# Kernel optimization log

Measured on AMD Instinct MI355X. Metric: run time of the kernel, lower is better.

## Reference

```python
import jax, jax.numpy as jnp
import numpy as np

B, N, DIM, HEADS, FFN, H, W = 8, 100, 256, 8, 2048, 128, 128
M = H * W
HD = DIM // HEADS
EPS = 1e-5


def ln(x, g, b):
    mu = jnp.mean(x, axis=-1, keepdims=True)
    var = jnp.mean(jnp.square(x - mu), axis=-1, keepdims=True)
    return (x - mu) * jax.lax.rsqrt(var + EPS) * g + b


def setup_inputs() -> dict:
    key = jax.random.key(0)
    ks = jax.random.split(key, 20)
    w = lambda k, shape: jax.random.normal(k, shape, jnp.float32) * 0.02
    inp = {
        "x": jax.random.normal(ks[0], (B, N, DIM), jnp.float32),
        "context": jax.random.normal(ks[1], (B, M, DIM), jnp.float32),
        "mask": jax.random.randint(ks[2], (B, N, H, W), 0, 2, jnp.int32),
        # masked cross-attention params
        "mq_w": w(ks[3], (DIM, DIM)), "mq_b": jnp.zeros((DIM,), jnp.float32),
        "mkv_w": w(ks[4], (2 * DIM, DIM)), "mkv_b": jnp.zeros((2 * DIM,), jnp.float32),
        "mproj_w": w(ks[5], (DIM, DIM)), "mproj_b": jnp.zeros((DIM,), jnp.float32),
        # nn.MultiheadAttention params
        "in_w": w(ks[6], (3 * DIM, DIM)), "in_b": jnp.zeros((3 * DIM,), jnp.float32),
        "out_w": w(ks[7], (DIM, DIM)), "out_b": jnp.zeros((DIM,), jnp.float32),
        # FFN params
        "w1": w(ks[8], (FFN, DIM)), "b1": jnp.zeros((FFN,), jnp.float32),
        "w2": w(ks[9], (DIM, FFN)), "b2": jnp.zeros((DIM,), jnp.float32),
        # LayerNorm params
        "n1_g": jnp.ones((DIM,), jnp.float32), "n1_b": jnp.zeros((DIM,), jnp.float32),
        "n2_g": jnp.ones((DIM,), jnp.float32), "n2_b": jnp.zeros((DIM,), jnp.float32),
        "n3_g": jnp.ones((DIM,), jnp.float32), "n3_b": jnp.zeros((DIM,), jnp.float32),
        "n4_g": jnp.ones((DIM,), jnp.float32), "n4_b": jnp.zeros((DIM,), jnp.float32),
    }
    return inp


def reference(x, context, mask, mq_w, mq_b, mkv_w, mkv_b, mproj_w, mproj_b,
              in_w, in_b, out_w, out_b, w1, b1, w2, b2,
              n1_g, n1_b, n2_g, n2_b, n3_g, n3_b, n4_g, n4_b):
    b, n, _ = x.shape
    m = context.shape[1]
    scale = HD ** -0.5

    # ---- masked cross-attention (pre-norm1, residual) ----
    res = x
    y = ln(x, n1_g, n1_b)
    q = (y @ mq_w.T + mq_b).reshape(b, n, HEADS, HD).transpose(0, 2, 1, 3)        # [b,h,n,d]
    kv = (context @ mkv_w.T + mkv_b).reshape(b, m, 2, HEADS, HD)
    k = kv[:, :, 0].transpose(0, 2, 1, 3)                                         # [b,h,m,d]
    v = kv[:, :, 1].transpose(0, 2, 1, 3)
    dots = jnp.einsum('bhnd,bhmd->bhnm', q, k) * scale                            # [b,h,n,m]
    mflat = mask.reshape(b, n, m)[:, None]                                        # [b,1,n,m]
    dots = jnp.where(mflat == 0, -jnp.inf, dots)
    attn = jax.nn.softmax(dots, axis=-1)
    o = jnp.einsum('bhnm,bhmd->bhnd', attn, v).transpose(0, 2, 1, 3).reshape(b, n, DIM)
    x = res + (o @ mproj_w.T + mproj_b)

    # ---- self-attention: torch MHA without batch_first, so seq axis = b, batch axis = n ----
    res = x
    y = ln(x, n2_g, n2_b)
    qkv = y @ in_w.T + in_b                                                       # [b,n,3*dim]
    sq, sk, sv = jnp.split(qkv, 3, axis=-1)
    sq = sq.reshape(b, n, HEADS, HD) * scale
    sk = sk.reshape(b, n, HEADS, HD)
    sv = sv.reshape(b, n, HEADS, HD)
    satt = jax.nn.softmax(jnp.einsum('inhd,jnhd->nhij', sq, sk), axis=-1)         # attn over seq=b
    so = jnp.einsum('nhij,jnhd->inhd', satt, sv).reshape(b, n, DIM)
    x = res + (so @ out_w.T + out_b)

    # ---- FFN ----
    res = x
    y = ln(x, n3_g, n3_b)
    f = jax.nn.gelu(y @ w1.T + b1, approximate=False) @ w2.T + b2
    x = res + f

    return ln(x, n4_g, n4_b)
```

## Files before the change

kernel.cpp:

```cpp
#include <hip/hip_runtime.h>
#include <hip/hip_bf16.h>

#define BB 8
#define NN 100
#define DIMM 256
#define HEADSS 8
#define HDD 32
#define FFNN 2048
#define MM 16384
#define ROWS (BB*NN)
#define CTX_ROWS (BB*MM)
#define SCALE 0.17677669529663689f

typedef __attribute__((ext_vector_type(8))) short s16x8;
typedef __attribute__((ext_vector_type(4))) float f32x4;

__device__ inline ushort f2bf(float f) {
    union { float f; unsigned u; } c; c.f = f;
    unsigned r = c.u + 0x7fffu + ((c.u >> 16) & 1u);
    return (ushort)(r >> 16);
}
__device__ inline float bf2f(ushort u) {
    union { unsigned i; float f; } c; c.i = ((unsigned)u) << 16; return c.f;
}

__global__ void ln_kernel(const float* __restrict__ x, const float* __restrict__ g,
                          const float* __restrict__ beta, float* __restrict__ y) {
    int row = blockIdx.x;
    int t = threadIdx.x;
    float v = x[row * 256 + t];
    __shared__ float red[256];
    red[t] = v; __syncthreads();
    for (int s = 128; s > 0; s >>= 1) { if (t < s) red[t] += red[t + s]; __syncthreads(); }
    float mu = red[0] * (1.0f / 256.0f);
    __syncthreads();
    float d = v - mu;
    red[t] = d * d; __syncthreads();
    for (int s = 128; s > 0; s >>= 1) { if (t < s) red[t] += red[t + s]; __syncthreads(); }
    float var = red[0] * (1.0f / 256.0f);
    float r = rsqrtf(var + 1e-5f);
    y[row * 256 + t] = d * r * g[t] + beta[t];
}

template<bool GELU, bool RES>
__global__ __launch_bounds__(256) void gemm_proj(const float* __restrict__ A,
                                                 const float* __restrict__ W,
                                                 const float* __restrict__ bias,
                                                 const float* __restrict__ res,
                                                 float* __restrict__ out,
                                                 int M, int K, int C) {
    int bm = blockIdx.x, bn = blockIdx.y;
    __shared__ __align__(16) ushort As[64 * 64];
    __shared__ __align__(16) ushort Bs[64 * 64];
    int t = threadIdx.x;
    int lane = t & 63, w = t >> 6;
    int wr = w >> 1, wc = w & 1;
    int l15 = lane & 15, lk = lane >> 4;
    int l7 = l15 & 7;

    f32x4 acc[2][2];
    #pragma unroll
    for (int i = 0; i < 2; i++)
        #pragma unroll
        for (int j = 0; j < 2; j++)
            acc[i][j] = (f32x4){0.f, 0.f, 0.f, 0.f};

    int srow = t >> 2;
    int sg0 = (t & 3) * 2;
    int swz0 = (sg0 ^ (srow & 7)) * 8;
    int swz1 = ((sg0 + 1) ^ (srow & 7)) * 8;
    int scol = sg0 * 8;

    int nkt = K >> 6;
    for (int kt = 0; kt < nkt; ++kt) {
        int kb = kt * 64 + scol;
        {
            int gr = bm * 64 + srow;
            s16x8 va0 = {0,0,0,0,0,0,0,0}, va1 = {0,0,0,0,0,0,0,0};
            if (gr < M) {
                const float* ap = A + (size_t)gr * K + kb;
                float4 a0 = *(const float4*)ap;
                float4 a1 = *(const float4*)(ap + 4);
                float4 a2 = *(const float4*)(ap + 8);
                float4 a3 = *(const float4*)(ap + 12);
                va0[0] = (short)f2bf(a0.x); va0[1] = (short)f2bf(a0.y);
                va0[2] = (short)f2bf(a0.z); va0[3] = (short)f2bf(a0.w);
                va0[4] = (short)f2bf(a1.x); va0[5] = (short)f2bf(a1.y);
                va0[6] = (short)f2bf(a1.z); va0[7] = (short)f2bf(a1.w);
                va1[0] = (short)f2bf(a2.x); va1[1] = (short)f2bf(a2.y);
                va1[2] = (short)f2bf(a2.z); va1[3] = (short)f2bf(a2.w);
                va1[4] = (short)f2bf(a3.x); va1[5] = (short)f2bf(a3.y);
                va1[6] = (short)f2bf(a3.z); va1[7] = (short)f2bf(a3.w);
            }
            *(s16x8*)&As[srow * 64 + swz0] = va0;
            *(s16x8*)&As[srow * 64 + swz1] = va1;
            const float* bp = W + (size_t)(bn * 64 + srow) * K + kb;
            float4 b0 = *(const float4*)bp;
            float4 b1 = *(const float4*)(bp + 4);
            float4 b2 = *(const float4*)(bp + 8);
            float4 b3 = *(const float4*)(bp + 12);
            s16x8 vb0, vb1;
            vb0[0] = (short)f2bf(b0.x); vb0[1] = (short)f2bf(b0.y);
            vb0[2] = (short)f2bf(b0.z); vb0[3] = (short)f2bf(b0.w);
            vb0[4] = (short)f2bf(b1.x); vb0[5] = (short)f2bf(b1.y);
            vb0[6] = (short)f2bf(b1.z); vb0[7] = (short)f2bf(b1.w);
            vb1[0] = (short)f2bf(b2.x); vb1[1] = (short)f2bf(b2.y);
            vb1[2] = (short)f2bf(b2.z); vb1[3] = (short)f2bf(b2.w);
            vb1[4] = (short)f2bf(b3.x); vb1[5] = (short)f2bf(b3.y);
            vb1[6] = (short)f2bf(b3.z); vb1[7] = (short)f2bf(b3.w);
            *(s16x8*)&Bs[srow * 64 + swz0] = vb0;
            *(s16x8*)&Bs[srow * 64 + swz1] = vb1;
        }
        __syncthreads();
        #pragma unroll
        for (int kk = 0; kk < 64; kk += 32) {
            int gsw = (((kk >> 3) + lk) ^ l7) * 8;
            s16x8 af[2], bf[2];
            #pragma unroll
            for (int mi = 0; mi < 2; mi++)
                af[mi] = *(const s16x8*)&As[(wr * 32 + mi * 16 + l15) * 64 + gsw];
            #pragma unroll
            for (int ni = 0; ni < 2; ni++)
                bf[ni] = *(const s16x8*)&Bs[(wc * 32 + ni * 16 + l15) * 64 + gsw];
            #pragma unroll
            for (int mi = 0; mi < 2; mi++)
                #pragma unroll
                for (int ni = 0; ni < 2; ni++)
                    acc[mi][ni] = __builtin_amdgcn_mfma_f32_16x16x32_bf16(af[mi], bf[ni], acc[mi][ni], 0, 0, 0);
        }
        __syncthreads();
    }
    #pragma unroll
    for (int ni = 0; ni < 2; ni++) {
        int col = bn * 64 + wc * 32 + ni * 16 + l15;
        float bv = bias[col];
        #pragma unroll
        for (int mi = 0; mi < 2; mi++) {
            int row0 = bm * 64 + wr * 32 + mi * 16 + lk * 4;
            #pragma unroll
            for (int r = 0; r < 4; r++) {
                int gr = row0 + r;
                if (gr < M) {
                    float v = acc[mi][ni][r] + bv;
                    if (GELU) v = 0.5f * v * (1.0f + erff(v * 0.70710678118654752f));
                    if (RES)  v += res[(size_t)gr * C + col];
                    out[(size_t)gr * C + col] = v;
                }
            }
        }
    }
}

__global__ __launch_bounds__(256) void gemm_kv(const float* __restrict__ A,
                                               const float* __restrict__ W,
                                               const float* __restrict__ bias,
                                               ushort* __restrict__ Kh,
                                               ushort* __restrict__ Vh) {
    int bn = blockIdx.x;
    int bm = blockIdx.y;
    __shared__ __align__(16) ushort As[128 * 64];
    __shared__ __align__(16) ushort Bs[128 * 64];
    int t = threadIdx.x;
    int lane = t & 63;
    int w = t >> 6;
    int wr = w >> 1, wc = w & 1;
    int l15 = lane & 15, lk = lane >> 4;
    int l7 = l15 & 7;

    f32x4 acc[4][4];
    #pragma unroll
    for (int i = 0; i < 4; i++)
        #pragma unroll
        for (int j = 0; j < 4; j++)
            acc[i][j] = (f32x4){0.f, 0.f, 0.f, 0.f};

    int srow = t >> 3;
    int sg   = t & 7;
    int skk  = sg * 8;
    int swz  = (sg ^ (srow & 7)) * 8;

    for (int kt = 0; kt < 4; ++kt) {
        int kbase = kt * 64;
        #pragma unroll
        for (int pass = 0; pass < 4; ++pass) {
            int row = pass * 32 + srow;
            const float* ap = A + (size_t)(bm * 128 + row) * 256 + kbase + skk;
            const float* bp = W + (size_t)(bn * 128 + row) * 256 + kbase + skk;
            float4 a0 = *(const float4*)ap;
            float4 a1 = *(const float4*)(ap + 4);
            float4 b0 = *(const float4*)bp;
            float4 b1 = *(const float4*)(bp + 4);
            s16x8 va, vb;
            va[0] = (short)f2bf(a0.x); va[1] = (short)f2bf(a0.y);
            va[2] = (short)f2bf(a0.z); va[3] = (short)f2bf(a0.w);
            va[4] = (short)f2bf(a1.x); va[5] = (short)f2bf(a1.y);
            va[6] = (short)f2bf(a1.z); va[7] = (short)f2bf(a1.w);
            vb[0] = (short)f2bf(b0.x); vb[1] = (short)f2bf(b0.y);
            vb[2] = (short)f2bf(b0.z); vb[3] = (short)f2bf(b0.w);
            vb[4] = (short)f2bf(b1.x); vb[5] = (short)f2bf(b1.y);
            vb[6] = (short)f2bf(b1.z); vb[7] = (short)f2bf(b1.w);
            *(s16x8*)&As[row * 64 + swz] = va;
            *(s16x8*)&Bs[row * 64 + swz] = vb;
        }
        __syncthreads();
        #pragma unroll
        for (int kk = 0; kk < 64; kk += 32) {
            int gsw = (((kk >> 3) + lk) ^ l7) * 8;
            s16x8 af[4], bf[4];
            #pragma unroll
            for (int mi = 0; mi < 4; mi++)
                af[mi] = *(const s16x8*)&As[(wr * 64 + mi * 16 + l15) * 64 + gsw];
            #pragma unroll
            for (int ni = 0; ni < 4; ni++)
                bf[ni] = *(const s16x8*)&Bs[(wc * 64 + ni * 16 + l15) * 64 + gsw];
            #pragma unroll
            for (int mi = 0; mi < 4; mi++)
                #pragma unroll
                for (int ni = 0; ni < 4; ni++)
                    acc[mi][ni] = __builtin_amdgcn_mfma_f32_16x16x32_bf16(af[mi], bf[ni], acc[mi][ni], 0, 0, 0);
        }
        __syncthreads();
    }
    #pragma unroll
    for (int ni = 0; ni < 4; ni++) {
        int col = bn * 128 + wc * 64 + ni * 16 + l15;
        float bv = bias[col];
        int isV = col >> 8;
        int c2 = col & 255;
        int h = c2 >> 5, hd = c2 & 31;
        ushort* dst = isV ? Vh : Kh;
        #pragma unroll
        for (int mi = 0; mi < 4; mi++) {
            int row0 = bm * 128 + wr * 64 + mi * 16 + lk * 4;
            #pragma unroll
            for (int r = 0; r < 4; r++) {
                int gr = row0 + r;
                int b = gr >> 14, m = gr & 16383;
                dst[(((size_t)(b * 8 + h)) * 16384 + m) * 32 + hd] = f2bf(acc[mi][ni][r] + bv);
            }
        }
    }
}

__global__ __launch_bounds__(256) void pack_mask(const int* __restrict__ mask,
                                                 unsigned* __restrict__ Mb) {
    unsigned tid = blockIdx.x * 256 + threadIdx.x;
    int b = tid >> 21;
    int rem = tid & ((1u << 21) - 1);
    int n = rem >> 14;
    int m = rem & 16383;
    int mv = 0;
    if (n < 100) mv = mask[(((size_t)b * 100 + n) << 14) + m];
    unsigned long long bal = __ballot(mv != 0);
    if ((threadIdx.x & 63) == 0) {
        size_t widx = (((size_t)b * 128 + n) << 9) + (m >> 5);
        *(unsigned long long*)(Mb + widx) = bal;
    }
}

__global__ __launch_bounds__(256) void xattn_flash(
        const float* __restrict__ q,
        const ushort* __restrict__ Kh,
        const ushort* __restrict__ Vh,
        const unsigned* __restrict__ Mb,
        float* __restrict__ O_part,
        float* __restrict__ m_part,
        float* __restrict__ l_part) {
    int ch = blockIdx.x;
    int h = blockIdx.y, b = blockIdx.z;
    int t = threadIdx.x;
    int lane = t & 63, w = t >> 6;
    int l15 = lane & 15, g = lane >> 4;

    __shared__ __align__(16) ushort Qs[128 * 40];
    __shared__ __align__(16) ushort Ks[64 * 40];
    __shared__ __align__(16) ushort Vt[32 * 72];
    __shared__ __align__(16) ushort Ps[128 * 72];
    __shared__ unsigned Ms[128 * 64];

    {
        int r = t >> 1, dh = (t & 1) * 16;
        s16x8 v0 = {0,0,0,0,0,0,0,0}, v1 = {0,0,0,0,0,0,0,0};
        if (r < 100) {
            const float* qp = q + ((size_t)(b * 100 + r)) * 256 + h * 32 + dh;
            #pragma unroll
            for (int j = 0; j < 8; j++) v0[j] = (short)f2bf(qp[j] * SCALE);
            #pragma unroll
            for (int j = 0; j < 8; j++) v1[j] = (short)f2bf(qp[8 + j] * SCALE);
        }
        *(s16x8*)&Qs[r * 40 + dh] = v0;
        *(s16x8*)&Qs[r * 40 + dh + 8] = v1;
    }
    {
        const unsigned* mp = Mb + (((size_t)b * 128) << 9) + ch * 64;
        #pragma unroll
        for (int i = 0; i < 32; i++) {
            int idx = t + i * 256;
            int r = idx >> 6, wd = idx & 63;
            Ms[idx] = mp[((size_t)r << 9) + wd];
        }
    }
    __syncthreads();

    s16x8 aq[2];
    aq[0] = *(const s16x8*)&Qs[(w * 32 + l15) * 40 + g * 8];
    aq[1] = *(const s16x8*)&Qs[(w * 32 + 16 + l15) * 40 + g * 8];

    float m_run[2][4], l_run[2][4];
    f32x4 accO[2][2];
    #pragma unroll
    for (int qt = 0; qt < 2; qt++) {
        #pragma unroll
        for (int r = 0; r < 4; r++) { m_run[qt][r] = -1e30f; l_run[qt][r] = 0.f; }
        accO[qt][0] = (f32x4){0.f,0.f,0.f,0.f};
        accO[qt][1] = (f32x4){0.f,0.f,0.f,0.f};
    }

    const ushort* Kbase = Kh + (((size_t)(b * 8 + h)) * 16384 + (size_t)ch * 2048) * 32;
    const ushort* Vbase = Vh + (((size_t)(b * 8 + h)) * 16384 + (size_t)ch * 2048) * 32;

    for (int tile = 0; tile < 32; ++tile) {
        if (tile) __syncthreads();
        {
            int mrow = t >> 2, d0 = (t & 3) * 8;
            uint4 k4 = *(const uint4*)(Kbase + ((size_t)(tile * 64 + mrow)) * 32 + d0);
            *(uint4*)&Ks[mrow * 40 + d0] = k4;
            uint4 v4 = *(const uint4*)(Vbase + ((size_t)(tile * 64 + mrow)) * 32 + d0);
            const ushort* vsp = (const ushort*)&v4;
            #pragma unroll
            for (int j = 0; j < 8; j++) Vt[(d0 + j) * 72 + mrow] = vsp[j];
        }
        __syncthreads();

        s16x8 bk[4];
        #pragma unroll
        for (int ni = 0; ni < 4; ni++)
            bk[ni] = *(const s16x8*)&Ks[(ni * 16 + l15) * 40 + g * 8];
        f32x4 sfrag[2][4];
        #pragma unroll
        for (int qt = 0; qt < 2; qt++)
            #pragma unroll
            for (int ni = 0; ni < 4; ni++)
                sfrag[qt][ni] = __builtin_amdgcn_mfma_f32_16x16x32_bf16(
                    aq[qt], bk[ni], (f32x4){0.f,0.f,0.f,0.f}, 0, 0, 0);

        #pragma unroll
        for (int qt = 0; qt < 2; qt++) {
            #pragma unroll
            for (int r = 0; r < 4; r++) {
                int qrow = w * 32 + qt * 16 + g * 4 + r;
                unsigned wd0 = Ms[qrow * 64 + tile * 2];
                unsigned wd1 = Ms[qrow * 64 + tile * 2 + 1];
                float sv[4];
                float mx = -1e30f;
                #pragma unroll
                for (int ni = 0; ni < 4; ni++) {
                    unsigned wdx = (ni < 2) ? wd0 : wd1;
                    unsigned bit = (wdx >> ((ni & 1) * 16 + l15)) & 1u;
                    sv[ni] = bit ? sfrag[qt][ni][r] : -1e30f;
                    mx = fmaxf(mx, sv[ni]);
                }
                mx = fmaxf(mx, __shfl_xor(mx, 1));
                mx = fmaxf(mx, __shfl_xor(mx, 2));
                mx = fmaxf(mx, __shfl_xor(mx, 4));
                mx = fmaxf(mx, __shfl_xor(mx, 8));
                float mnew = fmaxf(m_run[qt][r], mx);
                float corr = __expf(m_run[qt][r] - mnew);
                m_run[qt][r] = mnew;
                float rowsum = 0.f;
                #pragma unroll
                for (int ni = 0; ni < 4; ni++) {
                    float pv = __expf(sv[ni] - mnew);
                    rowsum += pv;
                    Ps[qrow * 72 + ni * 16 + l15] = f2bf(pv);
                }
                rowsum += __shfl_xor(rowsum, 1);
                rowsum += __shfl_xor(rowsum, 2);
                rowsum += __shfl_xor(rowsum, 4);
                rowsum += __shfl_xor(rowsum, 8);
                l_run[qt][r] = l_run[qt][r] * corr + rowsum;
                accO[qt][0][r] *= corr;
                accO[qt][1][r] *= corr;
            }
        }

        s16x8 ap0[2], ap1[2], bv0[2], bv1[2];
        #pragma unroll
        for (int qt = 0; qt < 2; qt++) {
            ap0[qt] = *(const s16x8*)&Ps[(w * 32 + qt * 16 + l15) * 72 + g * 8];
            ap1[qt] = *(const s16x8*)&Ps[(w * 32 + qt * 16 + l15) * 72 + 32 + g * 8];
        }
        #pragma unroll
        for (int dt = 0; dt < 2; dt++) {
            bv0[dt] = *(const s16x8*)&Vt[(dt * 16 + l15) * 72 + g * 8];
            bv1[dt] = *(const s16x8*)&Vt[(dt * 16 + l15) * 72 + 32 + g * 8];
        }
        #pragma unroll
        for (int qt = 0; qt < 2; qt++)
            #pragma unroll
            for (int dt = 0; dt < 2; dt++) {
                accO[qt][dt] = __builtin_amdgcn_mfma_f32_16x16x32_bf16(ap0[qt], bv0[dt], accO[qt][dt], 0, 0, 0);
                accO[qt][dt] = __builtin_amdgcn_mfma_f32_16x16x32_bf16(ap1[qt], bv1[dt], accO[qt][dt], 0, 0, 0);
            }
    }

    size_t pbase = ((size_t)(b * 8 + h) * 8 + ch) * 128;
    #pragma unroll
    for (int qt = 0; qt < 2; qt++) {
        #pragma unroll
        for (int r = 0; r < 4; r++) {
            int qrow = w * 32 + qt * 16 + g * 4 + r;
            #pragma unroll
            for (int dt = 0; dt < 2; dt++)
                O_part[(pbase + qrow) * 32 + dt * 16 + l15] = accO[qt][dt][r];
            if (l15 == 0) {
                m_part[pbase + qrow] = m_run[qt][r];
                l_part[pbase + qrow] = l_run[qt][r];
            }
        }
    }
}

__global__ __launch_bounds__(256) void xattn_combine(
        const float* __restrict__ O_part, const float* __restrict__ m_part,
        const float* __restrict__ l_part, float* __restrict__ o) {
    int n = blockIdx.x;
    int b = blockIdx.y;
    int t = threadIdx.x;
    int h = t >> 5, d = t & 31;
    size_t base = ((size_t)(b * 8 + h)) * 8;
    float gm = -1e30f;
    #pragma unroll
    for (int ch = 0; ch < 8; ch++)
        gm = fmaxf(gm, m_part[(base + ch) * 128 + n]);
    float L = 0.f, acc = 0.f;
    #pragma unroll
    for (int ch = 0; ch < 8; ch++) {
        float e = __expf(m_part[(base + ch) * 128 + n] - gm);
        L += l_part[(base + ch) * 128 + n] * e;
        acc += O_part[((base + ch) * 128 + n) * 32 + d] * e;
    }
    o[((size_t)(b * 100 + n)) * 256 + t] = acc / L;
}

__global__ void sattn_kernel(const float* __restrict__ qkv, float* __restrict__ so) {
    int n = blockIdx.x;
    int t = threadIdx.x;
    __shared__ float sq[8][256], sk[8][256], sv[8][256];
    __shared__ float S[512];
    for (int idx = t; idx < 8 * 768; idx += 256) {
        int i = idx / 768, c = idx - i * 768;
        float v = qkv[((size_t)(i * NN + n)) * 768 + c];
        if (c < 256) sq[i][c] = v * SCALE;
        else if (c < 512) sk[i][c - 256] = v;
        else sv[i][c - 512] = v;
    }
    __syncthreads();
    for (int idx = t; idx < 512; idx += 256) {
        int h = idx >> 6, i = (idx >> 3) & 7, j = idx & 7;
        float acc = 0.0f;
        #pragma unroll
        for (int d = 0; d < 32; d++) acc += sq[i][h * 32 + d] * sk[j][h * 32 + d];
        S[idx] = acc;
    }
    __syncthreads();
    if (t < 64) {
        int h = t >> 3, i = t & 7;
        float* row = &S[h * 64 + i * 8];
        float mx = row[0];
        #pragma unroll
        for (int j = 1; j < 8; j++) mx = fmaxf(mx, row[j]);
        float sum = 0.0f;
        #pragma unroll
        for (int j = 0; j < 8; j++) { row[j] = __expf(row[j] - mx); sum += row[j]; }
        float inv = 1.0f / sum;
        #pragma unroll
        for (int j = 0; j < 8; j++) row[j] *= inv;
    }
    __syncthreads();
    int c = t, h = t >> 5;
    #pragma unroll
    for (int i = 0; i < 8; i++) {
        float acc = 0.0f;
        #pragma unroll
        for (int j = 0; j < 8; j++) acc += S[h * 64 + i * 8 + j] * sv[j][c];
        so[((size_t)(i * NN + n)) * 256 + c] = acc;
    }
}

extern "C" void kernel_launch(void* const* d_in, const int* in_sizes, int n_in,
                              void* d_out, int out_size, void* d_ws, size_t ws_size,
                              hipStream_t stream) {
    const float* x      = (const float*)d_in[0];
    const float* ctx    = (const float*)d_in[1];
    const int*   mask   = (const int*)  d_in[2];
    const float* mq_w   = (const float*)d_in[3];
    const float* mq_b   = (const float*)d_in[4];
    const float* mkv_w  = (const float*)d_in[5];
    const float* mkv_b  = (const float*)d_in[6];
    const float* mproj_w= (const float*)d_in[7];
    const float* mproj_b= (const float*)d_in[8];
    const float* in_w   = (const float*)d_in[9];
    const float* in_b   = (const float*)d_in[10];
    const float* out_w  = (const float*)d_in[11];
    const float* out_b  = (const float*)d_in[12];
    const float* w1     = (const float*)d_in[13];
    const float* b1     = (const float*)d_in[14];
    const float* w2     = (const float*)d_in[15];
    const float* b2     = (const float*)d_in[16];
    const float* n1_g   = (const float*)d_in[17];
    const float* n1_b   = (const float*)d_in[18];
    const float* n2_g   = (const float*)d_in[19];
    const float* n2_b   = (const float*)d_in[20];
    const float* n3_g   = (const float*)d_in[21];
    const float* n3_b   = (const float*)d_in[22];
    const float* n4_g   = (const float*)d_in[23];
    const float* n4_b   = (const float*)d_in[24];

    float* ws = (float*)d_ws;
    float* Y1  = ws + 0;
    float* Q   = ws + 204800;
    float* O   = ws + 409600;
    float* X1  = ws + 614400;
    float* Y2  = ws + 819200;
    float* QKV = ws + 1024000;
    float* SO  = ws + 1638400;
    float* X2  = ws + 1843200;
    float* Y3  = ws + 2048000;
    float* F1  = ws + 2252800;
    float* X3  = ws + 3891200;
    unsigned* Mb     = (unsigned*)(ws + 819200);
    float*    O_part = ws + 1343488;
    float*    m_part = ws + 3440640;
    float*    l_part = ws + 3506176;
    ushort* Kh = (ushort*)((char*)d_ws + 16384000);
    ushort* Vh = (ushort*)((char*)d_ws + 16384000 + 67108864);

    float* out = (float*)d_out;

    ln_kernel<<<ROWS, 256, 0, stream>>>(x, n1_g, n1_b, Y1);
    gemm_proj<false, false><<<dim3(13, 4), 256, 0, stream>>>(
        Y1, mq_w, mq_b, nullptr, Q, ROWS, 256, 256);
    {
        dim3 grid(512 / 128, CTX_ROWS / 128);
        gemm_kv<<<grid, 256, 0, stream>>>(ctx, mkv_w, mkv_b, Kh, Vh);
    }
    pack_mask<<<(BB * 128 * MM) / 256, 256, 0, stream>>>(mask, Mb);
    {
        dim3 grid(8, HEADSS, BB);
        xattn_flash<<<grid, 256, 0, stream>>>(Q, Kh, Vh, Mb, O_part, m_part, l_part);
        dim3 cgrid(NN, BB);
        xattn_combine<<<cgrid, 256, 0, stream>>>(O_part, m_part, l_part, O);
    }
    gemm_proj<false, true><<<dim3(13, 4), 256, 0, stream>>>(
        O, mproj_w, mproj_b, x, X1, ROWS, 256, 256);
    ln_kernel<<<ROWS, 256, 0, stream>>>(X1, n2_g, n2_b, Y2);
    gemm_proj<false, false><<<dim3(13, 12), 256, 0, stream>>>(
        Y2, in_w, in_b, nullptr, QKV, ROWS, 256, 768);
    sattn_kernel<<<NN, 256, 0, stream>>>(QKV, SO);
    gemm_proj<false, true><<<dim3(13, 4), 256, 0, stream>>>(
        SO, out_w, out_b, X1, X2, ROWS, 256, 256);
    ln_kernel<<<ROWS, 256, 0, stream>>>(X2, n3_g, n3_b, Y3);
    gemm_proj<true, false><<<dim3(13, 32), 256, 0, stream>>>(
        Y3, w1, b1, nullptr, F1, ROWS, 256, FFNN);
    gemm_proj<false, true><<<dim3(13, 4), 256, 0, stream>>>(
        F1, w2, b2, X2, X3, ROWS, FFNN, 256);
    ln_kernel<<<ROWS, 256, 0, stream>>>(X3, n4_g, n4_b, out);
}
```

Measured before the change: 635.6 us.

## Pre-convert KV weights to bf16, prefetch tiles in registers, swizzle block order

```diff
diff --git a/kernel.cpp b/kernel.cpp
--- a/kernel.cpp
+++ b/kernel.cpp
@@ -22,6 +22,17 @@
 }
 __device__ inline float bf2f(ushort u) {
     union { unsigned i; float f; } c; c.i = ((unsigned)u) << 16; return c.f;
+}
+
+__global__ __launch_bounds__(256) void conv_bf16(const float* __restrict__ src,
+                                                 ushort* __restrict__ dst, int n4) {
+    int i = blockIdx.x * 256 + threadIdx.x;
+    if (i < n4) {
+        float4 v = ((const float4*)src)[i];
+        union { ushort u[4]; uint2 v2; } o;
+        o.u[0] = f2bf(v.x); o.u[1] = f2bf(v.y); o.u[2] = f2bf(v.z); o.u[3] = f2bf(v.w);
+        *(uint2*)&dst[i * 4] = o.v2;
+    }
 }
 
 __global__ void ln_kernel(const float* __restrict__ x, const float* __restrict__ g,
@@ -152,12 +163,13 @@
 }
 
 __global__ __launch_bounds__(256) void gemm_kv(const float* __restrict__ A,
-                                               const float* __restrict__ W,
+                                               const ushort* __restrict__ Wbf,
                                                const float* __restrict__ bias,
                                                ushort* __restrict__ Kh,
                                                ushort* __restrict__ Vh) {
-    int bn = blockIdx.x;
-    int bm = blockIdx.y;
+    int i = blockIdx.x;
+    int bm = ((i >> 5) << 3) + (i & 7);
+    int bn = (i >> 3) & 3;
     __shared__ __align__(16) ushort As[128 * 64];
     __shared__ __align__(16) ushort Bs[128 * 64];
     int t = threadIdx.x;
@@ -169,40 +181,58 @@
 
     f32x4 acc[4][4];
     #pragma unroll
-    for (int i = 0; i < 4; i++)
+    for (int ii = 0; ii < 4; ii++)
         #pragma unroll
         for (int j = 0; j < 4; j++)
-            acc[i][j] = (f32x4){0.f, 0.f, 0.f, 0.f};
+            acc[ii][j] = (f32x4){0.f, 0.f, 0.f, 0.f};
 
     int srow = t >> 3;
     int sg   = t & 7;
     int skk  = sg * 8;
     int swz  = (sg ^ (srow & 7)) * 8;
 
+    const float*  Abase = A   + (size_t)(bm * 128) * 256;
+    const ushort* Bbase = Wbf + (size_t)(bn * 128) * 256;
+
+    float4 ra[4][2];
+    uint4  rb[4];
+
+    {
+        int kbase = 0;
+        #pragma unroll
+        for (int p = 0; p < 4; p++) {
+            int row = p * 32 + srow;
+            const float* ap = Abase + (size_t)row * 256 + kbase + skk;
+            ra[p][0] = *(const float4*)ap;
+            ra[p][1] = *(const float4*)(ap + 4);
+            rb[p] = *(const uint4*)(Bbase + (size_t)row * 256 + kbase + skk);
+        }
+    }
+
     for (int kt = 0; kt < 4; ++kt) {
-        int kbase = kt * 64;
-        #pragma unroll
-        for (int pass = 0; pass < 4; ++pass) {
-            int row = pass * 32 + srow;
-            const float* ap = A + (size_t)(bm * 128 + row) * 256 + kbase + skk;
-            const float* bp = W + (size_t)(bn * 128 + row) * 256 + kbase + skk;
-            float4 a0 = *(const float4*)ap;
-            float4 a1 = *(const float4*)(ap + 4);
-            float4 b0 = *(const float4*)bp;
-            float4 b1 = *(const float4*)(bp + 4);
-            s16x8 va, vb;
-            va[0] = (short)f2bf(a0.x); va[1] = (short)f2bf(a0.y);
-            va[2] = (short)f2bf(a0.z); va[3] = (short)f2bf(a0.w);
-            va[4] = (short)f2bf(a1.x); va[5] = (short)f2bf(a1.y);
-            va[6] = (short)f2bf(a1.z); va[7] = (short)f2bf(a1.w);
-            vb[0] = (short)f2bf(b0.x); vb[1] = (short)f2bf(b0.y);
-            vb[2] = (short)f2bf(b0.z); vb[3] = (short)f2bf(b0.w);
-            vb[4] = (short)f2bf(b1.x); vb[5] = (short)f2bf(b1.y);
-            vb[6] = (short)f2bf(b1.z); vb[7] = (short)f2bf(b1.w);
+        #pragma unroll
+        for (int p = 0; p < 4; p++) {
+            int row = p * 32 + srow;
+            s16x8 va;
+            va[0] = (short)f2bf(ra[p][0].x); va[1] = (short)f2bf(ra[p][0].y);
+            va[2] = (short)f2bf(ra[p][0].z); va[3] = (short)f2bf(ra[p][0].w);
+            va[4] = (short)f2bf(ra[p][1].x); va[5] = (short)f2bf(ra[p][1].y);
+            va[6] = (short)f2bf(ra[p][1].z); va[7] = (short)f2bf(ra[p][1].w);
             *(s16x8*)&As[row * 64 + swz] = va;
-            *(s16x8*)&Bs[row * 64 + swz] = vb;
+            *(uint4*)&Bs[row * 64 + swz] = rb[p];
         }
         __syncthreads();
+        if (kt < 3) {
+            int kbase = (kt + 1) * 64;
+            #pragma unroll
+            for (int p = 0; p < 4; p++) {
+                int row = p * 32 + srow;
+                const float* ap = Abase + (size_t)row * 256 + kbase + skk;
+                ra[p][0] = *(const float4*)ap;
+                ra[p][1] = *(const float4*)(ap + 4);
+                rb[p] = *(const uint4*)(Bbase + (size_t)row * 256 + kbase + skk);
+            }
+        }
         #pragma unroll
         for (int kk = 0; kk < 64; kk += 32) {
             int gsw = (((kk >> 3) + lk) ^ l7) * 8;
@@ -533,6 +563,7 @@
     float*    O_part = ws + 1343488;
     float*    m_part = ws + 3440640;
     float*    l_part = ws + 3506176;
+    ushort*   Wkv_bf = (ushort*)(ws + 3571712);
     ushort* Kh = (ushort*)((char*)d_ws + 16384000);
     ushort* Vh = (ushort*)((char*)d_ws + 16384000 + 67108864);
 
@@ -541,10 +572,8 @@
     ln_kernel<<<ROWS, 256, 0, stream>>>(x, n1_g, n1_b, Y1);
     gemm_proj<false, false><<<dim3(13, 4), 256, 0, stream>>>(
         Y1, mq_w, mq_b, nullptr, Q, ROWS, 256, 256);
-    {
-        dim3 grid(512 / 128, CTX_ROWS / 128);
-        gemm_kv<<<grid, 256, 0, stream>>>(ctx, mkv_w, mkv_b, Kh, Vh);
-    }
+    conv_bf16<<<128, 256, 0, stream>>>(mkv_w, Wkv_bf, 32768);
+    gemm_kv<<<4096, 256, 0, stream>>>(ctx, Wkv_bf, mkv_b, Kh, Vh);
     pack_mask<<<(BB * 128 * MM) / 256, 256, 0, stream>>>(mask, Mb);
     {
         dim3 grid(8, HEADSS, BB);
```

After: 647.1 us. Within noise of the previous version (+1.8%).
